# Kernel optimization log

Hardware: AMD Instinct MI355X
Metric: run time of the kernel (lower is better)

## Reference

```python
import jax, jax.numpy as jnp
import numpy as np

WS = 8                 # window size (attn_grid_window_size)
N_WIN = WS * WS        # tokens per window = 64
EPS_LN = 1e-5

def _rel_index():
    # standard Swin/MaxViT relative position index for an 8x8 window
    coords = np.stack(np.meshgrid(np.arange(WS), np.arange(WS), indexing='ij')).reshape(2, -1)
    rel = coords[:, :, None] - coords[:, None, :]
    rel = rel.transpose(1, 2, 0).astype(np.int32)
    rel[..., 0] += WS - 1
    rel[..., 1] += WS - 1
    rel[..., 0] *= 2 * WS - 1
    return rel.sum(-1)  # [N_WIN, N_WIN] in [0, (2*WS-1)^2)

def layernorm(x, g, b):
    m = jnp.mean(x, -1, keepdims=True)
    v = jnp.mean((x - m) ** 2, -1, keepdims=True)
    return (x - m) * jax.lax.rsqrt(v + EPS_LN) * g + b

def l2norm(x):
    n = jnp.sqrt(jnp.sum(x * x, -1, keepdims=True))
    return x / jnp.maximum(n, 1e-12)  # torch F.normalize semantics

def setup_inputs() -> dict:
    key = jax.random.key(0)
    ks = jax.random.split(key, 4)
    B, C, H, W = 2, 256, 256, 256
    heads = 16
    s = 0.02
    return dict(
        X=jax.random.normal(ks[0], (B, C, H, W), jnp.float32),
        pre_g=jnp.ones((C,), jnp.float32), pre_b=jnp.zeros((C,), jnp.float32),
        post_g=jnp.ones((C,), jnp.float32), post_b=jnp.zeros((C,), jnp.float32),
        qkv_w=jax.random.normal(ks[1], (C, 3 * C), jnp.float32) * s,
        qkv_b=jnp.zeros((3 * C,), jnp.float32),
        proj_w=jax.random.normal(ks[2], (C, C), jnp.float32) * s,
        proj_b=jnp.zeros((C,), jnp.float32),
        rel_bias_table=jax.random.normal(ks[3], ((2 * WS - 1) ** 2, heads), jnp.float32) * s,
        rel_index=jnp.asarray(_rel_index()),
    )

def reference(X, pre_g, pre_b, post_g, post_b, qkv_w, qkv_b, proj_w, proj_b, rel_bias_table, rel_index):
    B, C, H, W = X.shape
    heads = rel_bias_table.shape[1]
    hd = C // heads
    # block partition: [B, C, H, W] -> [B*nH*nW, WS*WS, C]
    xw = X.reshape(B, C, H // WS, WS, W // WS, WS).transpose(0, 2, 4, 3, 5, 1)
    xw = xw.reshape(-1, N_WIN, C)
    Bw = xw.shape[0]
    # pre-norm + relative self-attention
    xn = layernorm(xw, pre_g, pre_b)
    qkv = (xn @ qkv_w + qkv_b).reshape(Bw, N_WIN, 3, heads, hd).transpose(2, 0, 3, 1, 4)
    q, k, v = qkv[0], qkv[1], qkv[2]            # [Bw, h, N, hd]
    q = l2norm(q)
    k = l2norm(k)                               # use_normalised_qk=True (MetNet-3)
    bias = rel_bias_table[rel_index.reshape(-1)].reshape(N_WIN, N_WIN, heads).transpose(2, 0, 1)
    attn = jax.nn.softmax(jnp.einsum('bhnd,bhmd->bhnm', q, k) + bias[None], axis=-1)
    out = jnp.einsum('bhnm,bhmd->bhnd', attn, v).transpose(0, 2, 1, 3).reshape(Bw, N_WIN, C)
    out = out @ proj_w + proj_b
    # residual, then post-norm branch (mlp = Identity)
    x = xw + out
    x = x + layernorm(x, post_g, post_b)
    # reverse partition -> [B, C, H, W]
    x = x.reshape(B, H // WS, W // WS, WS, WS, C).transpose(0, 5, 1, 3, 2, 4).reshape(B, C, H, W)
    return x
```

## Files before the change

### kernel.cpp

```cpp
#include <hip/hip_runtime.h>
#include <stdint.h>

typedef unsigned short u16;
typedef unsigned int   u32;

typedef short s8v __attribute__((ext_vector_type(8)));
typedef short s4v __attribute__((ext_vector_type(4)));
typedef float f4v __attribute__((ext_vector_type(4)));

struct __align__(8) US4 { u16 x, y, z, w; };

__device__ __forceinline__ u16 f2bf(float f) {
    union { float f; u32 u; } v; v.f = f;
    u32 u = v.u;
    return (u16)((u + 0x7fffu + ((u >> 16) & 1u)) >> 16);
}

#define MFMA16(a, b, c) __builtin_amdgcn_mfma_f32_16x16x16bf16_1k((a), (b), (c), 0, 0, 0)
#define MFMA32(a, b, c) __builtin_amdgcn_mfma_f32_16x16x32_bf16((a), (b), (c), 0, 0, 0)

__global__ void pack_kernel(const float* __restrict__ qkv_w, const float* __restrict__ proj_w,
                            const float* __restrict__ table, const int* __restrict__ ridx,
                            u16* __restrict__ pkQ, u16* __restrict__ pkP, float* __restrict__ biasP)
{
    int tid = blockIdx.x * 256 + threadIdx.x;
    if (tid < 24576) {
        int g = tid;
        int lane = g & 63, ks = (g >> 6) & 7, mt = g >> 9;
        int quad = lane >> 4, c = lane & 15;
        union { u16 h[8]; s8v v; } tmp;
#pragma unroll
        for (int j = 0; j < 8; ++j) {
            int kk = ks * 32 + quad * 8 + j;
            tmp.h[j] = f2bf(qkv_w[kk * 768 + mt * 16 + c]);
        }
        *(s8v*)&pkQ[g * 8] = tmp.v;
    } else if (tid < 32768) {
        int g = tid - 24576;
        int lane = g & 63, ks = (g >> 6) & 7, mt = g >> 9;
        int quad = lane >> 4, c = lane & 15;
        union { u16 h[8]; s8v v; } tmp;
#pragma unroll
        for (int j = 0; j < 8; ++j) {
            int kk = ks * 32 + quad * 8 + j;
            tmp.h[j] = f2bf(proj_w[kk * 256 + mt * 16 + c]);
        }
        *(s8v*)&pkP[g * 8] = tmp.v;
    } else if (tid < 49152) {
        int g = tid - 32768;
        int h = g >> 10, rest = (g >> 6) & 15, lane = g & 63;
        int mt = rest >> 2, nt = rest & 3;
        int quad = lane >> 4, c = lane & 15;
        int query = nt * 16 + c;
#pragma unroll
        for (int r = 0; r < 4; ++r) {
            int key = mt * 16 + quad * 4 + r;
            biasP[g * 4 + r] = table[ridx[query * 64 + key] * 16 + h];
        }
    }
}

__global__ __launch_bounds__(512, 4)
void attn_win_kernel(const float* __restrict__ X,
                     const float* __restrict__ pre_g, const float* __restrict__ pre_b,
                     const float* __restrict__ post_g, const float* __restrict__ post_b,
                     const float* __restrict__ qkv_b, const float* __restrict__ proj_b,
                     const u16* __restrict__ pkQ, const u16* __restrict__ pkP,
                     const float* __restrict__ biasP,
                     float* __restrict__ out)
{
    __shared__ __align__(16) unsigned char smem[75264];
    u16*   xnS = (u16*)smem;
    u16*   vS  = (u16*)(smem + 33792);
    float* xf  = (float*)smem;
    float* pst = (float*)(smem + 70656);
    float* st  = (float*)(smem + 74752);

    const int tid  = threadIdx.x;
    const int w    = tid >> 6;
    const int l    = tid & 63;
    const int quad = l >> 4;
    const int cc   = l & 15;

    const int bidx = blockIdx.x;
    const int win  = ((bidx & 7) << 8) | (bidx >> 3);
    const int bb = win >> 10;
    const int wh = (win >> 5) & 31;
    const int ww = win & 31;
    const size_t base = (((size_t)bb * 256) * 256 + wh * 8) * 256 + ww * 8;

    const int ch0 = tid >> 4;
    const int t0  = (tid & 15) * 4;
    const int r0  = t0 >> 3, c0 = t0 & 7;

    f4v xv[8];
#pragma unroll
    for (int it = 0; it < 8; ++it) {
        int ch = it * 32 + ch0;
        xv[it] = *(const f4v*)(X + base + (size_t)ch * 65536 + r0 * 256 + c0);
    }

    {
        float s[4] = {0.f,0.f,0.f,0.f}, ss[4] = {0.f,0.f,0.f,0.f};
#pragma unroll
        for (int it = 0; it < 8; ++it)
#pragma unroll
            for (int j = 0; j < 4; ++j) { float x = xv[it][j]; s[j] += x; ss[j] += x * x; }
#pragma unroll
        for (int j = 0; j < 4; ++j) {
            s[j]  += __shfl_xor(s[j], 16, 64);  s[j]  += __shfl_xor(s[j], 32, 64);
            ss[j] += __shfl_xor(ss[j], 16, 64); ss[j] += __shfl_xor(ss[j], 32, 64);
        }
        if (quad == 0) {
#pragma unroll
            for (int j = 0; j < 4; ++j) {
                pst[(w * 64 + t0 + j) * 2]     = s[j];
                pst[(w * 64 + t0 + j) * 2 + 1] = ss[j];
            }
        }
    }
    __syncthreads();
    if (tid < 64) {
        float S = 0.f, SS = 0.f;
#pragma unroll
        for (int wv = 0; wv < 8; ++wv) {
            S  += pst[(wv * 64 + tid) * 2];
            SS += pst[(wv * 64 + tid) * 2 + 1];
        }
        float mean = S * (1.f / 256.f);
        float var  = SS * (1.f / 256.f) - mean * mean;
        st[tid * 2] = mean; st[tid * 2 + 1] = rsqrtf(var + 1e-5f);
    }
    __syncthreads();

    {
        float mean[4], rstd[4];
#pragma unroll
        for (int j = 0; j < 4; ++j) { mean[j] = st[(t0 + j) * 2]; rstd[j] = st[(t0 + j) * 2 + 1]; }
#pragma unroll
        for (int it = 0; it < 8; ++it) {
            int ch = it * 32 + ch0;
            float g = pre_g[ch], b = pre_b[ch];
            u16 m0 = f2bf((xv[it][0] - mean[0]) * rstd[0] * g + b);
            u16 m1 = f2bf((xv[it][1] - mean[1]) * rstd[1] * g + b);
            u16 m2 = f2bf((xv[it][2] - mean[2]) * rstd[2] * g + b);
            u16 m3 = f2bf((xv[it][3] - mean[3]) * rstd[3] * g + b);
            u32 m01 = (u32)m0 | ((u32)m1 << 16);
            u32 m23 = (u32)m2 | ((u32)m3 << 16);
            u32 p01 = __shfl_xor(m01, 16, 64);
            u32 p23 = __shfl_xor(m23, 16, 64);
            if ((quad & 1) == 0) {
                *(u32*)&xnS[(t0 + 0) * 264 + ch] = (m01 & 0xffffu) | ((p01 & 0xffffu) << 16);
                *(u32*)&xnS[(t0 + 1) * 264 + ch] = (m01 >> 16)    | (p01 & 0xffff0000u);
            } else {
                *(u32*)&xnS[(t0 + 2) * 264 + ch - 1] = (p23 & 0xffffu) | ((m23 & 0xffffu) << 16);
                *(u32*)&xnS[(t0 + 3) * 264 + ch - 1] = (p23 >> 16)    | (m23 & 0xffff0000u);
            }
        }
    }
    __syncthreads();

    US4 outbuf[2][4];
    const s8v* AQ = (const s8v*)pkQ;
#pragma unroll
    for (int hi = 0; hi < 2; ++hi) {
        const int head = w * 2 + hi;
        s4v qfr[4], kfr[4];
        {
            f4v acc0[4], acc1[4], acc2[4];
#pragma unroll
            for (int nt = 0; nt < 4; ++nt) { acc0[nt] = 0.f; acc1[nt] = 0.f; acc2[nt] = 0.f; }
#pragma unroll
            for (int ks = 0; ks < 8; ++ks) {
                s8v bfr[4];
#pragma unroll
                for (int nt = 0; nt < 4; ++nt)
                    bfr[nt] = *(const s8v*)&xnS[(nt * 16 + cc) * 264 + ks * 32 + quad * 8];
                s8v a0 = AQ[((head     ) * 8 + ks) * 64 + l];
                s8v a1 = AQ[((head + 16) * 8 + ks) * 64 + l];
                s8v a2 = AQ[((head + 32) * 8 + ks) * 64 + l];
#pragma unroll
                for (int nt = 0; nt < 4; ++nt) {
                    acc0[nt] = MFMA32(a0, bfr[nt], acc0[nt]);
                    acc1[nt] = MFMA32(a1, bfr[nt], acc1[nt]);
                    acc2[nt] = MFMA32(a2, bfr[nt], acc2[nt]);
                }
            }
            {
                float b0 = qkv_b[head * 16 + quad * 4 + 0];
                float b1 = qkv_b[head * 16 + quad * 4 + 1];
                float b2 = qkv_b[head * 16 + quad * 4 + 2];
                float b3 = qkv_b[head * 16 + quad * 4 + 3];
#pragma unroll
                for (int nt = 0; nt < 4; ++nt) {
                    f4v a = acc0[nt];
                    a[0] += b0; a[1] += b1; a[2] += b2; a[3] += b3;
                    float sq = a[0]*a[0] + a[1]*a[1] + a[2]*a[2] + a[3]*a[3];
                    sq += __shfl_xor(sq, 16, 64);
                    sq += __shfl_xor(sq, 32, 64);
                    float inv = 1.0f / fmaxf(sqrtf(sq), 1e-12f);
                    s4v f;
                    f[0] = (short)f2bf(a[0] * inv); f[1] = (short)f2bf(a[1] * inv);
                    f[2] = (short)f2bf(a[2] * inv); f[3] = (short)f2bf(a[3] * inv);
                    qfr[nt] = f;
                }
            }
            {
                float b0 = qkv_b[(head + 16) * 16 + quad * 4 + 0];
                float b1 = qkv_b[(head + 16) * 16 + quad * 4 + 1];
                float b2 = qkv_b[(head + 16) * 16 + quad * 4 + 2];
                float b3 = qkv_b[(head + 16) * 16 + quad * 4 + 3];
#pragma unroll
                for (int nt = 0; nt < 4; ++nt) {
                    f4v a = acc1[nt];
                    a[0] += b0; a[1] += b1; a[2] += b2; a[3] += b3;
                    float sq = a[0]*a[0] + a[1]*a[1] + a[2]*a[2] + a[3]*a[3];
                    sq += __shfl_xor(sq, 16, 64);
                    sq += __shfl_xor(sq, 32, 64);
                    float inv = 1.0f / fmaxf(sqrtf(sq), 1e-12f);
                    s4v f;
                    f[0] = (short)f2bf(a[0] * inv); f[1] = (short)f2bf(a[1] * inv);
                    f[2] = (short)f2bf(a[2] * inv); f[3] = (short)f2bf(a[3] * inv);
                    kfr[nt] = f;
                }
            }
            {
                float b0 = qkv_b[(head + 32) * 16 + quad * 4 + 0];
                float b1 = qkv_b[(head + 32) * 16 + quad * 4 + 1];
                float b2 = qkv_b[(head + 32) * 16 + quad * 4 + 2];
                float b3 = qkv_b[(head + 32) * 16 + quad * 4 + 3];
                int chb = head * 16 + quad * 4;
#pragma unroll
                for (int nt = 0; nt < 4; ++nt) {
                    f4v a = acc2[nt];
                    a[0] += b0; a[1] += b1; a[2] += b2; a[3] += b3;
                    int tok = nt * 16 + cc;
                    float p0 = __shfl_xor(a[0], 1, 64), p1 = __shfl_xor(a[1], 1, 64);
                    float p2 = __shfl_xor(a[2], 1, 64), p3 = __shfl_xor(a[3], 1, 64);
                    if ((l & 1) == 0) {
                        *(u32*)&vS[(chb + 0) * 72 + tok] = (u32)f2bf(a[0]) | ((u32)f2bf(p0) << 16);
                        *(u32*)&vS[(chb + 1) * 72 + tok] = (u32)f2bf(a[1]) | ((u32)f2bf(p1) << 16);
                    } else {
                        *(u32*)&vS[(chb + 2) * 72 + tok - 1] = (u32)f2bf(p2) | ((u32)f2bf(a[2]) << 16);
                        *(u32*)&vS[(chb + 3) * 72 + tok - 1] = (u32)f2bf(p3) | ((u32)f2bf(a[3]) << 16);
                    }
                }
            }
        }
        {
            s4v vfr[4];
#pragma unroll
            for (int kt = 0; kt < 4; ++kt)
                vfr[kt] = *(const s4v*)&vS[(head * 16 + cc) * 72 + kt * 16 + quad * 4];
            const f4v* BP = (const f4v*)biasP;
#pragma unroll
            for (int half = 0; half < 2; ++half) {
                f4v sT[4][2];
#pragma unroll
                for (int nt2 = 0; nt2 < 2; ++nt2) {
                    int nt = half * 2 + nt2;
#pragma unroll
                    for (int mt = 0; mt < 4; ++mt)
                        sT[mt][nt2] = MFMA16(kfr[mt], qfr[nt], BP[(head * 16 + mt * 4 + nt) * 64 + l]);
                }
#pragma unroll
                for (int nt2 = 0; nt2 < 2; ++nt2) {
                    int nt = half * 2 + nt2;
                    float mx = -1e30f;
#pragma unroll
                    for (int mt = 0; mt < 4; ++mt)
#pragma unroll
                        for (int r = 0; r < 4; ++r) mx = fmaxf(mx, sT[mt][nt2][r]);
                    mx = fmaxf(mx, __shfl_xor(mx, 16, 64));
                    mx = fmaxf(mx, __shfl_xor(mx, 32, 64));
                    float p[16];
                    float sum = 0.f;
#pragma unroll
                    for (int mt = 0; mt < 4; ++mt)
#pragma unroll
                        for (int r = 0; r < 4; ++r) {
                            float e = __expf(sT[mt][nt2][r] - mx);
                            p[mt * 4 + r] = e; sum += e;
                        }
                    sum += __shfl_xor(sum, 16, 64);
                    sum += __shfl_xor(sum, 32, 64);
                    float inv = 1.f / sum;
                    f4v o = 0.f;
#pragma unroll
                    for (int kt = 0; kt < 4; ++kt) {
                        s4v pv = { (short)f2bf(p[kt * 4 + 0] * inv), (short)f2bf(p[kt * 4 + 1] * inv),
                                   (short)f2bf(p[kt * 4 + 2] * inv), (short)f2bf(p[kt * 4 + 3] * inv) };
                        o = MFMA16(vfr[kt], pv, o);
                    }
                    US4 ov; ov.x = f2bf(o[0]); ov.y = f2bf(o[1]); ov.z = f2bf(o[2]); ov.w = f2bf(o[3]);
                    outbuf[hi][nt] = ov;
                }
            }
        }
    }
    __syncthreads();
#pragma unroll
    for (int hi = 0; hi < 2; ++hi)
#pragma unroll
        for (int nt = 0; nt < 4; ++nt)
            *(US4*)&xnS[(nt * 16 + cc) * 264 + (w * 2 + hi) * 16 + quad * 4] = outbuf[hi][nt];
    __syncthreads();

    f4v xv2[8];
#pragma unroll
    for (int it = 0; it < 8; ++it) {
        int ch = it * 32 + ch0;
        xv2[it] = *(const f4v*)(X + base + (size_t)ch * 65536 + r0 * 256 + c0);
    }
    f4v pa0[4], pa1[4];
#pragma unroll
    for (int nt = 0; nt < 4; ++nt) { pa0[nt] = 0.f; pa1[nt] = 0.f; }
    {
        const s8v* AP = (const s8v*)pkP;
#pragma unroll
        for (int ks = 0; ks < 8; ++ks) {
            s8v bfr[4];
#pragma unroll
            for (int nt = 0; nt < 4; ++nt)
                bfr[nt] = *(const s8v*)&xnS[(nt * 16 + cc) * 264 + ks * 32 + quad * 8];
            s8v a0 = AP[((w * 2    ) * 8 + ks) * 64 + l];
            s8v a1 = AP[((w * 2 + 1) * 8 + ks) * 64 + l];
#pragma unroll
            for (int nt = 0; nt < 4; ++nt) {
                pa0[nt] = MFMA32(a0, bfr[nt], pa0[nt]);
                pa1[nt] = MFMA32(a1, bfr[nt], pa1[nt]);
            }
        }
    }
    __syncthreads();
    {
        int chb0 = (w * 2    ) * 16 + quad * 4;
        int chb1 = (w * 2 + 1) * 16 + quad * 4;
        float c00 = proj_b[chb0 + 0], c01 = proj_b[chb0 + 1], c02 = proj_b[chb0 + 2], c03 = proj_b[chb0 + 3];
        float c10 = proj_b[chb1 + 0], c11 = proj_b[chb1 + 1], c12 = proj_b[chb1 + 2], c13 = proj_b[chb1 + 3];
#pragma unroll
        for (int nt = 0; nt < 4; ++nt) {
            int tok = nt * 16 + cc;
            xf[(chb0 + 0) * 68 + tok] = pa0[nt][0] + c00;
            xf[(chb0 + 1) * 68 + tok] = pa0[nt][1] + c01;
            xf[(chb0 + 2) * 68 + tok] = pa0[nt][2] + c02;
            xf[(chb0 + 3) * 68 + tok] = pa0[nt][3] + c03;
            xf[(chb1 + 0) * 68 + tok] = pa1[nt][0] + c10;
            xf[(chb1 + 1) * 68 + tok] = pa1[nt][1] + c11;
            xf[(chb1 + 2) * 68 + tok] = pa1[nt][2] + c12;
            xf[(chb1 + 3) * 68 + tok] = pa1[nt][3] + c13;
        }
    }
    __syncthreads();

    f4v yv[8];
    {
        float s[4] = {0.f,0.f,0.f,0.f}, ss[4] = {0.f,0.f,0.f,0.f};
#pragma unroll
        for (int it = 0; it < 8; ++it) {
            int ch = it * 32 + ch0;
            f4v o = *(const f4v*)&xf[ch * 68 + t0];
            f4v y = xv2[it] + o;
            yv[it] = y;
#pragma unroll
            for (int j = 0; j < 4; ++j) { s[j] += y[j]; ss[j] += y[j] * y[j]; }
        }
#pragma unroll
        for (int j = 0; j < 4; ++j) {
            s[j]  += __shfl_xor(s[j], 16, 64);  s[j]  += __shfl_xor(s[j], 32, 64);
            ss[j] += __shfl_xor(ss[j], 16, 64); ss[j] += __shfl_xor(ss[j], 32, 64);
        }
        if (quad == 0) {
#pragma unroll
            for (int j = 0; j < 4; ++j) {
                pst[(w * 64 + t0 + j) * 2]     = s[j];
                pst[(w * 64 + t0 + j) * 2 + 1] = ss[j];
            }
        }
    }
    __syncthreads();
    if (tid < 64) {
        float S = 0.f, SS = 0.f;
#pragma unroll
        for (int wv = 0; wv < 8; ++wv) {
            S  += pst[(wv * 64 + tid) * 2];
            SS += pst[(wv * 64 + tid) * 2 + 1];
        }
        float mean = S * (1.f / 256.f);
        float var  = SS * (1.f / 256.f) - mean * mean;
        st[tid * 2] = mean; st[tid * 2 + 1] = rsqrtf(var + 1e-5f);
    }
    __syncthreads();

    {
        float mean[4], rstd[4];
#pragma unroll
        for (int j = 0; j < 4; ++j) { mean[j] = st[(t0 + j) * 2]; rstd[j] = st[(t0 + j) * 2 + 1]; }
#pragma unroll
        for (int it = 0; it < 8; ++it) {
            int ch = it * 32 + ch0;
            float g = post_g[ch], b = post_b[ch];
            f4v y = yv[it], z;
#pragma unroll
            for (int j = 0; j < 4; ++j)
                z[j] = y[j] + (y[j] - mean[j]) * rstd[j] * g + b;
            *(f4v*)(out + base + (size_t)ch * 65536 + r0 * 256 + c0) = z;
        }
    }
}

extern "C" void kernel_launch(void* const* d_in, const int* in_sizes, int n_in,
                              void* d_out, int out_size, void* d_ws, size_t ws_size,
                              hipStream_t stream)
{
    const float* X      = (const float*)d_in[0];
    const float* pre_g  = (const float*)d_in[1];
    const float* pre_b  = (const float*)d_in[2];
    const float* post_g = (const float*)d_in[3];
    const float* post_b = (const float*)d_in[4];
    const float* qkv_w  = (const float*)d_in[5];
    const float* qkv_b  = (const float*)d_in[6];
    const float* proj_w = (const float*)d_in[7];
    const float* proj_b = (const float*)d_in[8];
    const float* table  = (const float*)d_in[9];
    const int*   ridx   = (const int*)d_in[10];

    u16*   pkQ   = (u16*)d_ws;
    u16*   pkP   = (u16*)((char*)d_ws + 393216);
    float* biasP = (float*)((char*)d_ws + 524288);

    pack_kernel<<<192, 256, 0, stream>>>(qkv_w, proj_w, table, ridx, pkQ, pkP, biasP);
    attn_win_kernel<<<2048, 512, 0, stream>>>(X, pre_g, pre_b, post_g, post_b,
                                              qkv_b, proj_b, pkQ, pkP, biasP,
                                              (float*)d_out);
}
```

Baseline: 422.4 us.

## Use 16 waves per window block with one head per wave

```diff
diff --git a/kernel.cpp b/kernel.cpp
--- a/kernel.cpp
+++ b/kernel.cpp
@@ -60,7 +60,7 @@
     }
 }
 
-__global__ __launch_bounds__(512, 4)
+__global__ __launch_bounds__(1024, 8)
 void attn_win_kernel(const float* __restrict__ X,
                      const float* __restrict__ pre_g, const float* __restrict__ pre_b,
                      const float* __restrict__ post_g, const float* __restrict__ post_b,
@@ -69,12 +69,12 @@
                      const float* __restrict__ biasP,
                      float* __restrict__ out)
 {
-    __shared__ __align__(16) unsigned char smem[75264];
+    __shared__ __align__(16) unsigned char smem[78336];
     u16*   xnS = (u16*)smem;
     u16*   vS  = (u16*)(smem + 33792);
     float* xf  = (float*)smem;
-    float* pst = (float*)(smem + 70656);
-    float* st  = (float*)(smem + 74752);
+    float* pst = (float*)(smem + 69632);
+    float* st  = (float*)(smem + 77824);
 
     const int tid  = threadIdx.x;
     const int w    = tid >> 6;
@@ -93,17 +93,19 @@
     const int t0  = (tid & 15) * 4;
     const int r0  = t0 >> 3, c0 = t0 & 7;
 
-    f4v xv[8];
-#pragma unroll
-    for (int it = 0; it < 8; ++it) {
-        int ch = it * 32 + ch0;
+    u16* vSw = vS + w * 1088;
+
+    f4v xv[4];
+#pragma unroll
+    for (int it = 0; it < 4; ++it) {
+        int ch = it * 64 + ch0;
         xv[it] = *(const f4v*)(X + base + (size_t)ch * 65536 + r0 * 256 + c0);
     }
 
     {
         float s[4] = {0.f,0.f,0.f,0.f}, ss[4] = {0.f,0.f,0.f,0.f};
 #pragma unroll
-        for (int it = 0; it < 8; ++it)
+        for (int it = 0; it < 4; ++it)
 #pragma unroll
             for (int j = 0; j < 4; ++j) { float x = xv[it][j]; s[j] += x; ss[j] += x * x; }
 #pragma unroll
@@ -123,7 +125,7 @@
     if (tid < 64) {
         float S = 0.f, SS = 0.f;
 #pragma unroll
-        for (int wv = 0; wv < 8; ++wv) {
+        for (int wv = 0; wv < 16; ++wv) {
             S  += pst[(wv * 64 + tid) * 2];
             SS += pst[(wv * 64 + tid) * 2 + 1];
         }
@@ -138,8 +140,8 @@
 #pragma unroll
         for (int j = 0; j < 4; ++j) { mean[j] = st[(t0 + j) * 2]; rstd[j] = st[(t0 + j) * 2 + 1]; }
 #pragma unroll
-        for (int it = 0; it < 8; ++it) {
-            int ch = it * 32 + ch0;
+        for (int it = 0; it < 4; ++it) {
+            int ch = it * 64 + ch0;
             float g = pre_g[ch], b = pre_b[ch];
             u16 m0 = f2bf((xv[it][0] - mean[0]) * rstd[0] * g + b);
             u16 m1 = f2bf((xv[it][1] - mean[1]) * rstd[1] * g + b);
@@ -160,16 +162,15 @@
     }
     __syncthreads();
 
-    US4 outbuf[2][4];
-    const s8v* AQ = (const s8v*)pkQ;
-#pragma unroll
-    for (int hi = 0; hi < 2; ++hi) {
-        const int head = w * 2 + hi;
+    US4 outbuf[4];
+    {
+        const int head = w;
         s4v qfr[4], kfr[4];
         {
             f4v acc0[4], acc1[4], acc2[4];
 #pragma unroll
             for (int nt = 0; nt < 4; ++nt) { acc0[nt] = 0.f; acc1[nt] = 0.f; acc2[nt] = 0.f; }
+            const s8v* AQ = (const s8v*)pkQ;
 #pragma unroll
             for (int ks = 0; ks < 8; ++ks) {
                 s8v bfr[4];
@@ -229,7 +230,6 @@
                 float b1 = qkv_b[(head + 32) * 16 + quad * 4 + 1];
                 float b2 = qkv_b[(head + 32) * 16 + quad * 4 + 2];
                 float b3 = qkv_b[(head + 32) * 16 + quad * 4 + 3];
-                int chb = head * 16 + quad * 4;
 #pragma unroll
                 for (int nt = 0; nt < 4; ++nt) {
                     f4v a = acc2[nt];
@@ -237,12 +237,13 @@
                     int tok = nt * 16 + cc;
                     float p0 = __shfl_xor(a[0], 1, 64), p1 = __shfl_xor(a[1], 1, 64);
                     float p2 = __shfl_xor(a[2], 1, 64), p3 = __shfl_xor(a[3], 1, 64);
+                    int rb = quad * 4;
                     if ((l & 1) == 0) {
-                        *(u32*)&vS[(chb + 0) * 72 + tok] = (u32)f2bf(a[0]) | ((u32)f2bf(p0) << 16);
-                        *(u32*)&vS[(chb + 1) * 72 + tok] = (u32)f2bf(a[1]) | ((u32)f2bf(p1) << 16);
+                        *(u32*)&vSw[(rb + 0) * 68 + tok] = (u32)f2bf(a[0]) | ((u32)f2bf(p0) << 16);
+                        *(u32*)&vSw[(rb + 1) * 68 + tok] = (u32)f2bf(a[1]) | ((u32)f2bf(p1) << 16);
                     } else {
-                        *(u32*)&vS[(chb + 2) * 72 + tok - 1] = (u32)f2bf(p2) | ((u32)f2bf(a[2]) << 16);
-                        *(u32*)&vS[(chb + 3) * 72 + tok - 1] = (u32)f2bf(p3) | ((u32)f2bf(a[3]) << 16);
+                        *(u32*)&vSw[(rb + 2) * 68 + tok - 1] = (u32)f2bf(p2) | ((u32)f2bf(a[2]) << 16);
+                        *(u32*)&vSw[(rb + 3) * 68 + tok - 1] = (u32)f2bf(p3) | ((u32)f2bf(a[3]) << 16);
                     }
                 }
             }
@@ -251,7 +252,7 @@
             s4v vfr[4];
 #pragma unroll
             for (int kt = 0; kt < 4; ++kt)
-                vfr[kt] = *(const s4v*)&vS[(head * 16 + cc) * 72 + kt * 16 + quad * 4];
+                vfr[kt] = *(const s4v*)&vSw[cc * 68 + kt * 16 + quad * 4];
             const f4v* BP = (const f4v*)biasP;
 #pragma unroll
             for (int half = 0; half < 2; ++half) {
@@ -293,72 +294,59 @@
                         o = MFMA16(vfr[kt], pv, o);
                     }
                     US4 ov; ov.x = f2bf(o[0]); ov.y = f2bf(o[1]); ov.z = f2bf(o[2]); ov.w = f2bf(o[3]);
-                    outbuf[hi][nt] = ov;
-                }
-            }
-        }
-    }
-    __syncthreads();
-#pragma unroll
-    for (int hi = 0; hi < 2; ++hi)
-#pragma unroll
-        for (int nt = 0; nt < 4; ++nt)
-            *(US4*)&xnS[(nt * 16 + cc) * 264 + (w * 2 + hi) * 16 + quad * 4] = outbuf[hi][nt];
-    __syncthreads();
-
-    f4v xv2[8];
-#pragma unroll
-    for (int it = 0; it < 8; ++it) {
-        int ch = it * 32 + ch0;
+                    outbuf[nt] = ov;
+                }
+            }
+        }
+    }
+    __syncthreads();
+#pragma unroll
+    for (int nt = 0; nt < 4; ++nt)
+        *(US4*)&xnS[(nt * 16 + cc) * 264 + w * 16 + quad * 4] = outbuf[nt];
+    __syncthreads();
+
+    f4v xv2[4];
+#pragma unroll
+    for (int it = 0; it < 4; ++it) {
+        int ch = it * 64 + ch0;
         xv2[it] = *(const f4v*)(X + base + (size_t)ch * 65536 + r0 * 256 + c0);
     }
-    f4v pa0[4], pa1[4];
-#pragma unroll
-    for (int nt = 0; nt < 4; ++nt) { pa0[nt] = 0.f; pa1[nt] = 0.f; }
+    f4v pa[4];
+#pragma unroll
+    for (int nt = 0; nt < 4; ++nt) pa[nt] = 0.f;
     {
         const s8v* AP = (const s8v*)pkP;
 #pragma unroll
         for (int ks = 0; ks < 8; ++ks) {
-            s8v bfr[4];
-#pragma unroll
-            for (int nt = 0; nt < 4; ++nt)
-                bfr[nt] = *(const s8v*)&xnS[(nt * 16 + cc) * 264 + ks * 32 + quad * 8];
-            s8v a0 = AP[((w * 2    ) * 8 + ks) * 64 + l];
-            s8v a1 = AP[((w * 2 + 1) * 8 + ks) * 64 + l];
+            s8v a0 = AP[(w * 8 + ks) * 64 + l];
 #pragma unroll
             for (int nt = 0; nt < 4; ++nt) {
-                pa0[nt] = MFMA32(a0, bfr[nt], pa0[nt]);
-                pa1[nt] = MFMA32(a1, bfr[nt], pa1[nt]);
-            }
-        }
-    }
-    __syncthreads();
-    {
-        int chb0 = (w * 2    ) * 16 + quad * 4;
-        int chb1 = (w * 2 + 1) * 16 + quad * 4;
-        float c00 = proj_b[chb0 + 0], c01 = proj_b[chb0 + 1], c02 = proj_b[chb0 + 2], c03 = proj_b[chb0 + 3];
-        float c10 = proj_b[chb1 + 0], c11 = proj_b[chb1 + 1], c12 = proj_b[chb1 + 2], c13 = proj_b[chb1 + 3];
+                s8v bfr = *(const s8v*)&xnS[(nt * 16 + cc) * 264 + ks * 32 + quad * 8];
+                pa[nt] = MFMA32(a0, bfr, pa[nt]);
+            }
+        }
+    }
+    __syncthreads();
+    {
+        int chb = w * 16 + quad * 4;
+        float c00 = proj_b[chb + 0], c01 = proj_b[chb + 1], c02 = proj_b[chb + 2], c03 = proj_b[chb + 3];
 #pragma unroll
         for (int nt = 0; nt < 4; ++nt) {
             int tok = nt * 16 + cc;
-            xf[(chb0 + 0) * 68 + tok] = pa0[nt][0] + c00;
-            xf[(chb0 + 1) * 68 + tok] = pa0[nt][1] + c01;
-            xf[(chb0 + 2) * 68 + tok] = pa0[nt][2] + c02;
-            xf[(chb0 + 3) * 68 + tok] = pa0[nt][3] + c03;
-            xf[(chb1 + 0) * 68 + tok] = pa1[nt][0] + c10;
-            xf[(chb1 + 1) * 68 + tok] = pa1[nt][1] + c11;
-            xf[(chb1 + 2) * 68 + tok] = pa1[nt][2] + c12;
-            xf[(chb1 + 3) * 68 + tok] = pa1[nt][3] + c13;
-        }
-    }
-    __syncthreads();
-
-    f4v yv[8];
+            xf[(chb + 0) * 68 + tok] = pa[nt][0] + c00;
+            xf[(chb + 1) * 68 + tok] = pa[nt][1] + c01;
+            xf[(chb + 2) * 68 + tok] = pa[nt][2] + c02;
+            xf[(chb + 3) * 68 + tok] = pa[nt][3] + c03;
+        }
+    }
+    __syncthreads();
+
+    f4v yv[4];
     {
         float s[4] = {0.f,0.f,0.f,0.f}, ss[4] = {0.f,0.f,0.f,0.f};
 #pragma unroll
-        for (int it = 0; it < 8; ++it) {
-            int ch = it * 32 + ch0;
+        for (int it = 0; it < 4; ++it) {
+            int ch = it * 64 + ch0;
             f4v o = *(const f4v*)&xf[ch * 68 + t0];
             f4v y = xv2[it] + o;
             yv[it] = y;
@@ -382,7 +370,7 @@
     if (tid < 64) {
         float S = 0.f, SS = 0.f;
 #pragma unroll
-        for (int wv = 0; wv < 8; ++wv) {
+        for (int wv = 0; wv < 16; ++wv) {
             S  += pst[(wv * 64 + tid) * 2];
             SS += pst[(wv * 64 + tid) * 2 + 1];
         }
@@ -397,8 +385,8 @@
 #pragma unroll
         for (int j = 0; j < 4; ++j) { mean[j] = st[(t0 + j) * 2]; rstd[j] = st[(t0 + j) * 2 + 1]; }
 #pragma unroll
-        for (int it = 0; it < 8; ++it) {
-            int ch = it * 32 + ch0;
+        for (int it = 0; it < 4; ++it) {
+            int ch = it * 64 + ch0;
             float g = post_g[ch], b = post_b[ch];
             f4v y = yv[it], z;
 #pragma unroll
@@ -430,7 +418,7 @@
     float* biasP = (float*)((char*)d_ws + 524288);
 
     pack_kernel<<<192, 256, 0, stream>>>(qkv_w, proj_w, table, ridx, pkQ, pkP, biasP);
-    attn_win_kernel<<<2048, 512, 0, stream>>>(X, pre_g, pre_b, post_g, post_b,
-                                              qkv_b, proj_b, pkQ, pkP, biasP,
-                                              (float*)d_out);
+    attn_win_kernel<<<2048, 1024, 0, stream>>>(X, pre_g, pre_b, post_g, post_b,
+                                               qkv_b, proj_b, pkQ, pkP, biasP,
+                                               (float*)d_out);
 }
```

Result: slower. 934.0 us (+121.1%).
